# Kernel optimization log

Measured on AMD Instinct MI355X. Metric: run time of the kernel, lower is better.

Reference implementation:

```python
import jax, jax.numpy as jnp
import numpy as np

MIN_LOGITS_VALUE = -2.3819763e+38
MAX_WAVELENGTH = 10000


def _apply_rope(inputs, positions):
    # inputs: [b, t, n, h]; positions: [b, t]. RoPE on first half of h.
    x_rope, x = jnp.split(inputs, 2, axis=-1)
    pos = positions[:, :, None, None].astype(jnp.float32)  # [b, t, 1, 1]
    freq_exponents = 2.0 * jnp.arange(x_rope.shape[-1] // 2) / x_rope.shape[-1]
    inv_freq = 1.0 / (MAX_WAVELENGTH ** freq_exponents)
    sinusoid = pos * inv_freq  # [b, t, 1, h/2]
    sin = jnp.sin(sinusoid).astype(inputs.dtype)
    cos = jnp.cos(sinusoid).astype(inputs.dtype)
    first, second = jnp.split(x_rope, 2, axis=-1)
    return jnp.concatenate(
        [first * cos - second * sin, second * cos + first * sin, x], axis=-1)


def _forward_pass_mask(segment_pos, window_size):
    # segment_pos: [b, t]; 0 marks a segment start.
    segment_ids = jnp.cumsum(segment_pos == 0, axis=-1)  # [b, t]
    t = segment_pos.shape[-1]
    positions = jnp.arange(t)
    same_segment = segment_ids[:, :, None] == segment_ids[:, None, :]
    causal = positions[:, None] >= positions[None, :]
    window = positions[:, None] <= positions[None, :] + window_size
    return same_segment & (causal & window)[None]  # [b, t, t]


def setup_inputs() -> dict:
    key = jax.random.key(0)
    ks = jax.random.split(key, 6)
    B, T, W, N = 2, 2048, 2048, 16
    H = W // N
    x = jax.random.normal(ks[0], (B, T, W), jnp.float32)
    sc = 1.0 / np.sqrt(W).astype(np.float32)
    w_q = jax.random.normal(ks[1], (W, W), jnp.float32) * sc
    w_k = jax.random.normal(ks[2], (W, H), jnp.float32) * sc
    w_v = jax.random.normal(ks[3], (W, H), jnp.float32) * sc
    w_out = jax.random.normal(ks[4], (W, W), jnp.float32) * sc
    b_out = jnp.zeros((W,), jnp.float32)
    segment_pos = jnp.tile(jnp.arange(T, dtype=jnp.int32)[None], (B, 1))
    return {"x": x, "w_q": w_q, "w_k": w_k, "w_v": w_v, "w_out": w_out,
            "b_out": b_out, "segment_pos": segment_pos,
            "num_heads": N, "window_size": 1024}


def reference(x, w_q, w_k, w_v, w_out, b_out, segment_pos, num_heads, window_size):
    b, t, width = x.shape
    head_dim = width // num_heads
    # Projections: MQA -> keys/values are single-head [b, t, head_dim].
    q = (x @ w_q).reshape(b, t, num_heads, head_dim)
    k = (x @ w_k)[:, :, None, :]  # [b, t, 1, h]
    v = x @ w_v                   # [b, t, h]
    q = _apply_rope(q, segment_pos)
    k = _apply_rope(k, segment_pos)[:, :, 0]  # [b, t, h]
    logits = jnp.einsum('btnh,bsh->bnts', q, k) * (head_dim ** -0.5)
    mask = _forward_pass_mask(segment_pos, window_size)  # [b, t, t]
    masked = jnp.where(mask[:, None], logits, MIN_LOGITS_VALUE).astype(jnp.float32)
    probs = jax.nn.softmax(masked, axis=-1).astype(x.dtype)
    encoded = jnp.einsum('bnts,bsh->btnh', probs, v).reshape(b, t, width)
    return encoded @ w_out + b_out
```

## Files before the change

kernel.cpp:

```cpp
#include <hip/hip_runtime.h>
#include <hip/hip_bf16.h>
#include <stdint.h>

typedef __attribute__((ext_vector_type(8))) short short8;
typedef __attribute__((ext_vector_type(4))) float f32x4;

__device__ __forceinline__ float bf2f(short u) {
  return __uint_as_float(((unsigned)(unsigned short)u) << 16);
}
__device__ __forceinline__ short f2bf(float f) {
  unsigned x = __float_as_uint(f);
  unsigned r = (x + 0x7fffu + ((x >> 16) & 1u)) >> 16;
  return (short)r;
}

__device__ __forceinline__ void gload_lds16(const short* g, short* l) {
  __builtin_amdgcn_global_load_lds(
      (const __attribute__((address_space(1))) void*)g,
      (__attribute__((address_space(3))) void*)l, 16, 0, 0);
}

__global__ void cast_x_bf16(const float* __restrict__ in, short* __restrict__ out, int n8) {
  int i = blockIdx.x * blockDim.x + threadIdx.x;
  if (i >= n8) return;
  const float4* p = (const float4*)in + (size_t)i * 2;
  float4 a = p[0], b = p[1];
  short8 o;
  o[0] = f2bf(a.x); o[1] = f2bf(a.y); o[2] = f2bf(a.z); o[3] = f2bf(a.w);
  o[4] = f2bf(b.x); o[5] = f2bf(b.y); o[6] = f2bf(b.z); o[7] = f2bf(b.w);
  *((short8*)out + i) = o;
}

__global__ void transpose_cast(const float* __restrict__ in, int R, int C,
                               short* __restrict__ out, int row_off, int ldo) {
  __shared__ float tile[32][33];
  int c0 = blockIdx.x * 32, r0 = blockIdx.y * 32;
  int tx = threadIdx.x, ty = threadIdx.y;
#pragma unroll
  for (int i = 0; i < 4; ++i)
    tile[ty + i * 8][tx] = in[(size_t)(r0 + ty + i * 8) * C + (c0 + tx)];
  __syncthreads();
#pragma unroll
  for (int i = 0; i < 4; ++i)
    out[(size_t)(row_off + c0 + ty + i * 8) * ldo + (r0 + tx)] =
        f2bf(tile[tx][ty + i * 8]);
}

template <int OUT_F32>
__global__ __launch_bounds__(256)
void gemm_bt(const short* __restrict__ A, const short* __restrict__ Bt,
             int M, int N, int K, int ldc,
             short* __restrict__ outb, float* __restrict__ outf,
             const float* __restrict__ bias) {
  __shared__ short As[128 * 64];
  __shared__ short Bs[128 * 64];
  const int tid = threadIdx.x, lane = tid & 63;
  const int wr = tid >> 7, wc = (tid >> 6) & 1;
  const int l15 = lane & 15, l4 = lane >> 4;
  const int m0 = blockIdx.y * 128, n0 = blockIdx.x * 128;
  f32x4 acc[4][4] = {};
  for (int k0 = 0; k0 < K; k0 += 64) {
#pragma unroll
    for (int iss = 0; iss < 4; ++iss) {
      int c = iss * 256 + tid;
      int row = c >> 3, q = c & 7;
      gload_lds16(A + (size_t)(m0 + row) * K + k0 + q * 8,
                  As + iss * 2048 + (tid & 192) * 8);
      gload_lds16(Bt + (size_t)(n0 + row) * K + k0 + q * 8,
                  Bs + iss * 2048 + (tid & 192) * 8);
    }
    __syncthreads();
#pragma unroll
    for (int kk = 0; kk < 2; ++kk) {
      short8 a[4], b[4];
#pragma unroll
      for (int mi = 0; mi < 4; ++mi)
        a[mi] = *(const short8*)(As + (wr * 64 + mi * 16 + l15) * 64 + kk * 32 + l4 * 8);
#pragma unroll
      for (int ni = 0; ni < 4; ++ni)
        b[ni] = *(const short8*)(Bs + (wc * 64 + ni * 16 + l15) * 64 + kk * 32 + l4 * 8);
#pragma unroll
      for (int mi = 0; mi < 4; ++mi)
#pragma unroll
        for (int ni = 0; ni < 4; ++ni)
          acc[mi][ni] = __builtin_amdgcn_mfma_f32_16x16x32_bf16(a[mi], b[ni], acc[mi][ni], 0, 0, 0);
    }
    __syncthreads();
  }
#pragma unroll
  for (int mi = 0; mi < 4; ++mi)
#pragma unroll
    for (int ni = 0; ni < 4; ++ni)
#pragma unroll
      for (int r = 0; r < 4; ++r) {
        int row = m0 + wr * 64 + mi * 16 + l4 * 4 + r;
        int col = n0 + wc * 64 + ni * 16 + l15;
        if (OUT_F32)
          outf[(size_t)row * ldc + col] = acc[mi][ni][r] + bias[col];
        else
          outb[(size_t)row * ldc + col] = f2bf(acc[mi][ni][r]);
      }
}

__global__ void rope_kernel(short* __restrict__ qkv, const int* __restrict__ segpos,
                            int nheads, int hd, int ld) {
  const int row = blockIdx.x;
  const float pos = (float)segpos[row];
  short* base = qkv + (size_t)row * ld;
  const int quarter = hd >> 2;
  const int npairs_q = nheads * quarter;
  const int total = npairs_q + quarter;
  for (int p = threadIdx.x; p < total; p += blockDim.x) {
    int i, off;
    if (p < npairs_q) { off = (p >> 5) * hd; i = p & 31; }
    else              { off = nheads * hd;  i = p - npairs_q; }
    float ang = pos * exp2f(-(float)i * (13.287712379549449f / (float)quarter));
    float s, c;
    sincosf(ang, &s, &c);
    float a = bf2f(base[off + i]);
    float b = bf2f(base[off + quarter + i]);
    base[off + i]           = f2bf(a * c - b * s);
    base[off + quarter + i] = f2bf(b * c + a * s);
  }
}

#define SWZV(h) ((((h) ^ ((h) >> 3)) & 7) << 4)
__global__ __launch_bounds__(512)
void attn_kernel(const short* __restrict__ qkv, short* __restrict__ enc,
                 const int* __restrict__ wsz_p, int T, int nheads, int nqt, int bhc) {
  const int window = wsz_p[0];
  const int i = blockIdx.x;
  const int qt = nqt - 1 - (i / bhc);
  const int bh = i % bhc;
  const int b = bh / nheads, n = bh % nheads;
  const int tid = threadIdx.x, lane = tid & 63, w = tid >> 6;
  const int l15 = lane & 15, l4 = lane >> 4;
  const int q0 = qt * 128;
  const size_t rowbase = (size_t)b * T;
  const int LD = nheads * 128 + 256;
  const int kcol = nheads * 128;
  const float CC = 0.08838834764831845f * 1.4426950408889634f;

  __shared__ short Ks[64 * 128];
  __shared__ short Vt[128 * 64];
  __shared__ short Pl[8][16 * 72];

  short8 qf[4];
  {
    const short* qptr = qkv + (rowbase + q0 + w * 16 + l15) * LD + n * 128 + l4 * 8;
#pragma unroll
    for (int kk = 0; kk < 4; ++kk) qf[kk] = *(const short8*)(qptr + kk * 32);
  }
  f32x4 o[8] = {};
  float mrow[4], lrow[4];
#pragma unroll
  for (int r = 0; r < 4; ++r) { mrow[r] = -1e30f; lrow[r] = 0.f; }

  const int tmin = q0 + w * 16, tmax = tmin + 15;
  int st_lo = q0 - window; if (st_lo < 0) st_lo = 0; st_lo >>= 6;
  const int st_hi = (q0 + 127) >> 6;

  short8 kreg[2], vreg[2];
  auto load_tile = [&](int s0) {
#pragma unroll
    for (int it = 0; it < 2; ++it) {
      int c = it * 512 + tid;
      int r = c >> 4, cg = c & 15;
      const short* rowp = qkv + (rowbase + s0 + r) * (size_t)LD + kcol;
      kreg[it] = *(const short8*)(rowp + cg * 8);
      vreg[it] = *(const short8*)(rowp + 128 + cg * 8);
    }
  };
  auto store_tile = [&]() {
#pragma unroll
    for (int it = 0; it < 2; ++it) {
      int c = it * 512 + tid;
      int r = c >> 4, cg = c & 15;
      *(short8*)((char*)Ks + ((r * 256 + cg * 16) ^ ((r & 7) << 4))) = kreg[it];
      int h0 = cg * 8;
#pragma unroll
      for (int j = 0; j < 8; ++j) {
        int h = h0 + j;
        *(short*)((char*)Vt + ((h * 128 + r * 2) ^ SWZV(h))) = vreg[it][j];
      }
    }
  };

  load_tile(st_lo * 64);
  store_tile();
  __syncthreads();

  for (int st = st_lo; st <= st_hi; ++st) {
    const int s0 = st * 64;
    const bool more = (st < st_hi);
    if (more) load_tile(s0 + 64);

    const bool active = (s0 <= tmax) && (tmin <= s0 + 63 + window);
    if (active) {
      f32x4 sacc[4];
      __builtin_amdgcn_s_setprio(1);
#pragma unroll
      for (int si = 0; si < 4; ++si) {
        f32x4 acc = {};
        int srow = si * 16 + l15;
#pragma unroll
        for (int kk = 0; kk < 4; ++kk) {
          int byt = (srow * 256 + (kk * 32 + l4 * 8) * 2) ^ ((srow & 7) << 4);
          short8 kf = *(const short8*)((const char*)Ks + byt);
          acc = __builtin_amdgcn_mfma_f32_16x16x32_bf16(qf[kk], kf, acc, 0, 0, 0);
        }
        sacc[si] = acc;
      }
      __builtin_amdgcn_s_setprio(0);

      const int trow0 = q0 + w * 16 + l4 * 4;
      float mt[4];
#pragma unroll
      for (int r = 0; r < 4; ++r) mt[r] = -1e30f;
#pragma unroll
      for (int si = 0; si < 4; ++si) {
        int s = s0 + si * 16 + l15;
#pragma unroll
        for (int r = 0; r < 4; ++r) {
          int t = trow0 + r;
          float v = (s <= t && t <= s + window) ? sacc[si][r] : -1e30f;
          sacc[si][r] = v;
          mt[r] = fmaxf(mt[r], v);
        }
      }
#pragma unroll
      for (int r = 0; r < 4; ++r)
#pragma unroll
        for (int off = 1; off < 16; off <<= 1)
          mt[r] = fmaxf(mt[r], __shfl_xor(mt[r], off));

      bool dfr = true;
#pragma unroll
      for (int r = 0; r < 4; ++r) dfr = dfr && ((mt[r] - mrow[r]) * CC <= 8.0f);
      const bool defer = __all(dfr);
      float fac[4];
      if (!defer) {
#pragma unroll
        for (int r = 0; r < 4; ++r) {
          float mnew = fmaxf(mrow[r], mt[r]);
          fac[r] = exp2f((mrow[r] - mnew) * CC);
          mrow[r] = mnew;
        }
      }
      float psum[4];
#pragma unroll
      for (int r = 0; r < 4; ++r) psum[r] = 0.f;
#pragma unroll
      for (int si = 0; si < 4; ++si)
#pragma unroll
        for (int r = 0; r < 4; ++r) {
          float p = exp2f((sacc[si][r] - mrow[r]) * CC);
          psum[r] += p;
          Pl[w][(l4 * 4 + r) * 72 + si * 16 + l15] = f2bf(p);
        }
#pragma unroll
      for (int r = 0; r < 4; ++r) {
#pragma unroll
        for (int off = 1; off < 16; off <<= 1)
          psum[r] += __shfl_xor(psum[r], off);
        if (!defer) lrow[r] = lrow[r] * fac[r] + psum[r];
        else        lrow[r] += psum[r];
      }
      if (!defer) {
#pragma unroll
        for (int nt = 0; nt < 8; ++nt)
#pragma unroll
          for (int r = 0; r < 4; ++r) o[nt][r] *= fac[r];
      }

      __builtin_amdgcn_s_setprio(1);
#pragma unroll
      for (int kk = 0; kk < 2; ++kk) {
        short8 pf = *(const short8*)(&Pl[w][l15 * 72 + kk * 32 + l4 * 8]);
#pragma unroll
        for (int nt = 0; nt < 8; ++nt) {
          int h = nt * 16 + l15;
          int vb = (h * 128 + kk * 64 + l4 * 16) ^ SWZV(h);
          short8 vf = *(const short8*)((const char*)Vt + vb);
          o[nt] = __builtin_amdgcn_mfma_f32_16x16x32_bf16(pf, vf, o[nt], 0, 0, 0);
        }
      }
      __builtin_amdgcn_s_setprio(0);
    }
    __syncthreads();
    if (more) store_tile();
    __syncthreads();
  }

#pragma unroll
  for (int nt = 0; nt < 8; ++nt)
#pragma unroll
    for (int r = 0; r < 4; ++r) {
      size_t row = rowbase + q0 + w * 16 + l4 * 4 + r;
      int col = n * 128 + nt * 16 + l15;
      enc[row * (size_t)(nheads * 128) + col] = f2bf(o[nt][r] / lrow[r]);
    }
}

extern "C" void kernel_launch(void* const* d_in, const int* in_sizes, int n_in,
                              void* d_out, int out_size, void* d_ws, size_t ws_size,
                              hipStream_t stream) {
  const float* x     = (const float*)d_in[0];
  const float* w_q   = (const float*)d_in[1];
  const float* w_k   = (const float*)d_in[2];
  const float* w_v   = (const float*)d_in[3];
  const float* w_out = (const float*)d_in[4];
  const float* b_out = (const float*)d_in[5];
  const int* segpos  = (const int*)d_in[6];
  const int* wsz     = (const int*)d_in[8];
  float* out = (float*)d_out;

  const int BT = in_sizes[6];
  const int W  = in_sizes[5];
  const int H  = in_sizes[2] / W;
  const int NH = W / H;
  const int T  = 2048;
  const int NQKV = W + 2 * H;

  char* ws = (char*)d_ws;
  short* xb    = (short*)ws;
  short* wqkvT = (short*)(ws + (size_t)BT * W * 2);
  short* woutT = (short*)(ws + (size_t)(BT * W + NQKV * W) * 2);
  short* qkv   = (short*)(ws + (size_t)(BT * W + NQKV * W + W * W) * 2);
  short* enc   = xb;

  int n8 = BT * W / 8;
  cast_x_bf16<<<(n8 + 255) / 256, 256, 0, stream>>>(x, xb, n8);

  dim3 tb(32, 8);
  transpose_cast<<<dim3(W / 32, W / 32), tb, 0, stream>>>(w_q, W, W, wqkvT, 0, W);
  transpose_cast<<<dim3(H / 32, W / 32), tb, 0, stream>>>(w_k, W, H, wqkvT, W, W);
  transpose_cast<<<dim3(H / 32, W / 32), tb, 0, stream>>>(w_v, W, H, wqkvT, W + H, W);
  transpose_cast<<<dim3(W / 32, W / 32), tb, 0, stream>>>(w_out, W, W, woutT, 0, W);

  gemm_bt<0><<<dim3(NQKV / 128, BT / 128), 256, 0, stream>>>(
      xb, wqkvT, BT, NQKV, W, NQKV, qkv, nullptr, nullptr);

  rope_kernel<<<BT, 256, 0, stream>>>(qkv, segpos, NH, H, NQKV);

  const int nqt = T / 128;
  const int bhc = (BT / T) * NH;
  attn_kernel<<<nqt * bhc, 512, 0, stream>>>(qkv, enc, wsz, T, NH, nqt, bhc);

  gemm_bt<1><<<dim3(W / 128, BT / 128), 256, 0, stream>>>(
      enc, woutT, BT, W, W, W, nullptr, out, b_out);
}
```

Measured before the change: 378.7 us.

## Use 256x256 double-buffered GEMM, pre-transpose V, skip masking on full tiles

Replaces the 128x128 single-buffered projection GEMM with a 256x256 tile, 512-thread kernel. It double-buffers LDS, XOR-swizzles LDS addresses and interleaves next-tile loads with MFMA phases, aiming for more data reuse and hidden load latency. A separate kernel transposes V into a [b, h, t] buffer so attention can store V tiles to LDS with vector writes instead of scalar scattered stores. Attention also skips per-element mask evaluation on tiles lying fully inside the causal window. The tradeoff is that the larger tiles give only 144 and 128 blocks for the two GEMMs, fewer than the CU count, so the GPU may be underfilled; the transpose adds one extra launch.

```diff
diff --git a/kernel.cpp b/kernel.cpp
--- a/kernel.cpp
+++ b/kernel.cpp
@@ -46,55 +46,137 @@
         f2bf(tile[tx][ty + i * 8]);
 }
 
+__global__ void transpose_v(const short* __restrict__ qkv, short* __restrict__ vT,
+                            int T, int LD, int vcol) {
+  __shared__ short tile[32][33];
+  int t0 = blockIdx.x * 32, h0 = blockIdx.y * 32, b = blockIdx.z;
+  int tx = threadIdx.x, ty = threadIdx.y;
+#pragma unroll
+  for (int i = 0; i < 4; ++i)
+    tile[ty + i * 8][tx] = qkv[((size_t)b * T + t0 + ty + i * 8) * LD + vcol + h0 + tx];
+  __syncthreads();
+#pragma unroll
+  for (int i = 0; i < 4; ++i)
+    vT[((size_t)b * 128 + h0 + ty + i * 8) * T + t0 + tx] = tile[tx][ty + i * 8];
+}
+
 template <int OUT_F32>
-__global__ __launch_bounds__(256)
-void gemm_bt(const short* __restrict__ A, const short* __restrict__ Bt,
+__global__ __launch_bounds__(512, 2)
+void gemm256(const short* __restrict__ A, const short* __restrict__ Bt,
              int M, int N, int K, int ldc,
              short* __restrict__ outb, float* __restrict__ outf,
              const float* __restrict__ bias) {
-  __shared__ short As[128 * 64];
-  __shared__ short Bs[128 * 64];
-  const int tid = threadIdx.x, lane = tid & 63;
-  const int wr = tid >> 7, wc = (tid >> 6) & 1;
+  __shared__ short As[2][256 * 64];
+  __shared__ short Bs[2][256 * 64];
+  const int tid = threadIdx.x, lane = tid & 63, w = tid >> 6;
+  const int wm = w >> 2, wn = w & 3;
   const int l15 = lane & 15, l4 = lane >> 4;
-  const int m0 = blockIdx.y * 128, n0 = blockIdx.x * 128;
-  f32x4 acc[4][4] = {};
-  for (int k0 = 0; k0 < K; k0 += 64) {
-#pragma unroll
-    for (int iss = 0; iss < 4; ++iss) {
-      int c = iss * 256 + tid;
-      int row = c >> 3, q = c & 7;
-      gload_lds16(A + (size_t)(m0 + row) * K + k0 + q * 8,
-                  As + iss * 2048 + (tid & 192) * 8);
-      gload_lds16(Bt + (size_t)(n0 + row) * K + k0 + q * 8,
-                  Bs + iss * 2048 + (tid & 192) * 8);
+  const int m0 = blockIdx.y * 256, n0 = blockIdx.x * 256;
+  const int sw = (l15 & 7) << 4;
+  const int NT = K / 64;
+
+  f32x4 acc[8][4] = {};
+  short8 a[4][2], b[4][2];
+
+  auto stage = [&](short* dst, const short* src, int base0, int k0) {
+#pragma unroll
+    for (int i = 0; i < 4; ++i) {
+      int chunk = i * 8 + w;
+      int r = chunk * 8 + (lane >> 3);
+      int cs = ((lane & 7) ^ ((lane >> 3) & 7)) * 8;
+      gload_lds16(src + (size_t)(base0 + r) * K + k0 + cs, dst + chunk * 512);
     }
-    __syncthreads();
-#pragma unroll
-    for (int kk = 0; kk < 2; ++kk) {
-      short8 a[4], b[4];
-#pragma unroll
-      for (int mi = 0; mi < 4; ++mi)
-        a[mi] = *(const short8*)(As + (wr * 64 + mi * 16 + l15) * 64 + kk * 32 + l4 * 8);
-#pragma unroll
-      for (int ni = 0; ni < 4; ++ni)
-        b[ni] = *(const short8*)(Bs + (wc * 64 + ni * 16 + l15) * 64 + kk * 32 + l4 * 8);
-#pragma unroll
-      for (int mi = 0; mi < 4; ++mi)
-#pragma unroll
-        for (int ni = 0; ni < 4; ++ni)
-          acc[mi][ni] = __builtin_amdgcn_mfma_f32_16x16x32_bf16(a[mi], b[ni], acc[mi][ni], 0, 0, 0);
-    }
-    __syncthreads();
+  };
+
+  auto rdA = [&](const short* buf, int mi, int kk) -> short8 {
+    int row = wm * 128 + mi * 16 + l15;
+    int byt = row * 128 + ((kk * 64 + l4 * 16) ^ sw);
+    return *(const short8*)((const char*)buf + byt);
+  };
+  auto rdB = [&](const short* buf, int ni, int kk) -> short8 {
+    int row = wn * 64 + ni * 16 + l15;
+    int byt = row * 128 + ((kk * 64 + l4 * 16) ^ sw);
+    return *(const short8*)((const char*)buf + byt);
+  };
+
+  stage(As[0], A, m0, 0);
+  stage(Bs[0], Bt, n0, 0);
+  asm volatile("s_waitcnt vmcnt(0)" ::: "memory");
+  __builtin_amdgcn_s_barrier();
+
+  for (int t = 0; t < NT; ++t) {
+    const int bf = t & 1, nb = bf ^ 1;
+    const bool pre = (t + 1 < NT);
+    const short* Ab = As[bf];
+    const short* Bb = Bs[bf];
+
+#pragma unroll
+    for (int mg = 0; mg < 4; ++mg) { a[mg][0] = rdA(Ab, mg, 0); a[mg][1] = rdA(Ab, mg, 1); }
+#pragma unroll
+    for (int ng = 0; ng < 2; ++ng) { b[ng][0] = rdB(Bb, ng, 0); b[ng][1] = rdB(Bb, ng, 1); }
+    if (pre) stage(As[nb], A, m0, (t + 1) * 64);
+    __builtin_amdgcn_s_barrier();
+    __builtin_amdgcn_s_setprio(1);
+#pragma unroll
+    for (int mg = 0; mg < 4; ++mg)
+#pragma unroll
+      for (int ng = 0; ng < 2; ++ng) {
+        acc[mg][ng] = __builtin_amdgcn_mfma_f32_16x16x32_bf16(a[mg][0], b[ng][0], acc[mg][ng], 0, 0, 0);
+        acc[mg][ng] = __builtin_amdgcn_mfma_f32_16x16x32_bf16(a[mg][1], b[ng][1], acc[mg][ng], 0, 0, 0);
+      }
+    __builtin_amdgcn_s_setprio(0);
+    __builtin_amdgcn_s_barrier();
+
+#pragma unroll
+    for (int ng = 2; ng < 4; ++ng) { b[ng][0] = rdB(Bb, ng, 0); b[ng][1] = rdB(Bb, ng, 1); }
+    if (pre) stage(Bs[nb], Bt, n0, (t + 1) * 64);
+    __builtin_amdgcn_s_barrier();
+    __builtin_amdgcn_s_setprio(1);
+#pragma unroll
+    for (int mg = 0; mg < 4; ++mg)
+#pragma unroll
+      for (int ng = 2; ng < 4; ++ng) {
+        acc[mg][ng] = __builtin_amdgcn_mfma_f32_16x16x32_bf16(a[mg][0], b[ng][0], acc[mg][ng], 0, 0, 0);
+        acc[mg][ng] = __builtin_amdgcn_mfma_f32_16x16x32_bf16(a[mg][1], b[ng][1], acc[mg][ng], 0, 0, 0);
+      }
+    __builtin_amdgcn_s_setprio(0);
+    __builtin_amdgcn_s_barrier();
+
+#pragma unroll
+    for (int mg = 0; mg < 4; ++mg) { a[mg][0] = rdA(Ab, mg + 4, 0); a[mg][1] = rdA(Ab, mg + 4, 1); }
+    __builtin_amdgcn_s_barrier();
+    __builtin_amdgcn_s_setprio(1);
+#pragma unroll
+    for (int mg = 0; mg < 4; ++mg)
+#pragma unroll
+      for (int ng = 0; ng < 2; ++ng) {
+        acc[mg + 4][ng] = __builtin_amdgcn_mfma_f32_16x16x32_bf16(a[mg][0], b[ng][0], acc[mg + 4][ng], 0, 0, 0);
+        acc[mg + 4][ng] = __builtin_amdgcn_mfma_f32_16x16x32_bf16(a[mg][1], b[ng][1], acc[mg + 4][ng], 0, 0, 0);
+      }
+    __builtin_amdgcn_s_setprio(0);
+    __builtin_amdgcn_s_barrier();
+
+    __builtin_amdgcn_s_setprio(1);
+#pragma unroll
+    for (int mg = 0; mg < 4; ++mg)
+#pragma unroll
+      for (int ng = 2; ng < 4; ++ng) {
+        acc[mg + 4][ng] = __builtin_amdgcn_mfma_f32_16x16x32_bf16(a[mg][0], b[ng][0], acc[mg + 4][ng], 0, 0, 0);
+        acc[mg + 4][ng] = __builtin_amdgcn_mfma_f32_16x16x32_bf16(a[mg][1], b[ng][1], acc[mg + 4][ng], 0, 0, 0);
+      }
+    __builtin_amdgcn_s_setprio(0);
+    asm volatile("s_waitcnt vmcnt(0)" ::: "memory");
+    __builtin_amdgcn_s_barrier();
   }
-#pragma unroll
-  for (int mi = 0; mi < 4; ++mi)
+
+#pragma unroll
+  for (int mi = 0; mi < 8; ++mi)
 #pragma unroll
     for (int ni = 0; ni < 4; ++ni)
 #pragma unroll
       for (int r = 0; r < 4; ++r) {
-        int row = m0 + wr * 64 + mi * 16 + l4 * 4 + r;
-        int col = n0 + wc * 64 + ni * 16 + l15;
+        int row = m0 + wm * 128 + mi * 16 + l4 * 4 + r;
+        int col = n0 + wn * 64 + ni * 16 + l15;
         if (OUT_F32)
           outf[(size_t)row * ldc + col] = acc[mi][ni][r] + bias[col];
         else
@@ -124,9 +206,9 @@
   }
 }
 
-#define SWZV(h) ((((h) ^ ((h) >> 3)) & 7) << 4)
 __global__ __launch_bounds__(512)
-void attn_kernel(const short* __restrict__ qkv, short* __restrict__ enc,
+void attn_kernel(const short* __restrict__ qkv, const short* __restrict__ vT,
+                 short* __restrict__ enc,
                  const int* __restrict__ wsz_p, int T, int nheads, int nqt, int bhc) {
   const int window = wsz_p[0];
   const int i = blockIdx.x;
@@ -165,24 +247,18 @@
 #pragma unroll
     for (int it = 0; it < 2; ++it) {
       int c = it * 512 + tid;
-      int r = c >> 4, cg = c & 15;
-      const short* rowp = qkv + (rowbase + s0 + r) * (size_t)LD + kcol;
-      kreg[it] = *(const short8*)(rowp + cg * 8);
-      vreg[it] = *(const short8*)(rowp + 128 + cg * 8);
+      kreg[it] = *(const short8*)(qkv + (rowbase + s0 + (c >> 4)) * (size_t)LD + kcol + (c & 15) * 8);
+      vreg[it] = *(const short8*)(vT + ((size_t)b * 128 + (c >> 3)) * T + s0 + (c & 7) * 8);
     }
   };
   auto store_tile = [&]() {
 #pragma unroll
     for (int it = 0; it < 2; ++it) {
       int c = it * 512 + tid;
-      int r = c >> 4, cg = c & 15;
-      *(short8*)((char*)Ks + ((r * 256 + cg * 16) ^ ((r & 7) << 4))) = kreg[it];
-      int h0 = cg * 8;
-#pragma unroll
-      for (int j = 0; j < 8; ++j) {
-        int h = h0 + j;
-        *(short*)((char*)Vt + ((h * 128 + r * 2) ^ SWZV(h))) = vreg[it][j];
-      }
+      int r = c >> 4;
+      *(short8*)((char*)Ks + ((r * 256 + (c & 15) * 16) ^ ((r & 7) << 4))) = kreg[it];
+      int h = c >> 3;
+      *(short8*)((char*)Vt + ((h * 128 + (c & 7) * 16) ^ ((h & 7) << 4))) = vreg[it];
     }
   };
 
@@ -214,18 +290,25 @@
       __builtin_amdgcn_s_setprio(0);
 
       const int trow0 = q0 + w * 16 + l4 * 4;
+      const bool full = (s0 + 63 <= tmin) && (tmax <= s0 + window);
       float mt[4];
-#pragma unroll
-      for (int r = 0; r < 4; ++r) mt[r] = -1e30f;
-#pragma unroll
-      for (int si = 0; si < 4; ++si) {
-        int s = s0 + si * 16 + l15;
-#pragma unroll
-        for (int r = 0; r < 4; ++r) {
-          int t = trow0 + r;
-          float v = (s <= t && t <= s + window) ? sacc[si][r] : -1e30f;
-          sacc[si][r] = v;
-          mt[r] = fmaxf(mt[r], v);
+      if (full) {
+#pragma unroll
+        for (int r = 0; r < 4; ++r)
+          mt[r] = fmaxf(fmaxf(sacc[0][r], sacc[1][r]), fmaxf(sacc[2][r], sacc[3][r]));
+      } else {
+#pragma unroll
+        for (int r = 0; r < 4; ++r) mt[r] = -1e30f;
+#pragma unroll
+        for (int si = 0; si < 4; ++si) {
+          int s = s0 + si * 16 + l15;
+#pragma unroll
+          for (int r = 0; r < 4; ++r) {
+            int t = trow0 + r;
+            float v = (s <= t && t <= s + window) ? sacc[si][r] : -1e30f;
+            sacc[si][r] = v;
+            mt[r] = fmaxf(mt[r], v);
+          }
         }
       }
 #pragma unroll
@@ -280,7 +363,7 @@
 #pragma unroll
         for (int nt = 0; nt < 8; ++nt) {
           int h = nt * 16 + l15;
-          int vb = (h * 128 + kk * 64 + l4 * 16) ^ SWZV(h);
+          int vb = (h * 128 + kk * 64 + l4 * 16) ^ ((h & 7) << 4);
           short8 vf = *(const short8*)((const char*)Vt + vb);
           o[nt] = __builtin_amdgcn_mfma_f32_16x16x32_bf16(pf, vf, o[nt], 0, 0, 0);
         }
@@ -320,6 +403,7 @@
   const int H  = in_sizes[2] / W;
   const int NH = W / H;
   const int T  = 2048;
+  const int B  = BT / T;
   const int NQKV = W + 2 * H;
 
   char* ws = (char*)d_ws;
@@ -327,6 +411,7 @@
   short* wqkvT = (short*)(ws + (size_t)BT * W * 2);
   short* woutT = (short*)(ws + (size_t)(BT * W + NQKV * W) * 2);
   short* qkv   = (short*)(ws + (size_t)(BT * W + NQKV * W + W * W) * 2);
+  short* vTp   = wqkvT;
   short* enc   = xb;
 
   int n8 = BT * W / 8;
@@ -338,15 +423,17 @@
   transpose_cast<<<dim3(H / 32, W / 32), tb, 0, stream>>>(w_v, W, H, wqkvT, W + H, W);
   transpose_cast<<<dim3(W / 32, W / 32), tb, 0, stream>>>(w_out, W, W, woutT, 0, W);
 
-  gemm_bt<0><<<dim3(NQKV / 128, BT / 128), 256, 0, stream>>>(
+  gemm256<0><<<dim3(NQKV / 256, BT / 256), 512, 0, stream>>>(
       xb, wqkvT, BT, NQKV, W, NQKV, qkv, nullptr, nullptr);
 
   rope_kernel<<<BT, 256, 0, stream>>>(qkv, segpos, NH, H, NQKV);
 
+  transpose_v<<<dim3(T / 32, H / 32, B), tb, 0, stream>>>(qkv, vTp, T, NQKV, NH * H + H);
+
   const int nqt = T / 128;
-  const int bhc = (BT / T) * NH;
-  attn_kernel<<<nqt * bhc, 512, 0, stream>>>(qkv, enc, wsz, T, NH, nqt, bhc);
-
-  gemm_bt<1><<<dim3(W / 128, BT / 128), 256, 0, stream>>>(
+  const int bhc = B * NH;
+  attn_kernel<<<nqt * bhc, 512, 0, stream>>>(qkv, vTp, enc, wsz, T, NH, nqt, bhc);
+
+  gemm256<1><<<dim3(W / 256, BT / 256), 512, 0, stream>>>(
       enc, woutT, BT, W, W, W, nullptr, out, b_out);
 }
```

After: 359.0 us. 5.2% less time.
